# Kernel optimization log

Measured on AMD Instinct MI355X. Metric: run time of the kernel, lower is better.

The kernel has to match this reference:

```python
import jax, jax.numpy as jnp
import numpy as np

N = 100000
E = 3200000
F_IN = 256
F_OUT = 256
HID = 64


def setup_inputs() -> dict:
    key = jax.random.key(0)
    ks = jax.random.split(key, 16)
    stdv = 1.0 / np.sqrt(F_OUT)
    std_att = 1.0 / np.sqrt(HID)
    std_att_vec = 1.0 / np.sqrt(3.0)
    u = lambda k, shape, s: jax.random.uniform(k, shape, jnp.float32, -s, s)
    return {
        "inputx": jax.random.normal(ks[0], (N, F_IN), jnp.float32),
        "row_A": jax.random.randint(ks[1], (E,), 0, N),
        "col_A": jax.random.randint(ks[2], (E,), 0, N),
        "val_A": jax.random.uniform(ks[3], (E,), jnp.float32),
        "row_A2": jax.random.randint(ks[4], (E,), 0, N),
        "col_A2": jax.random.randint(ks[5], (E,), 0, N),
        "val_A2": jax.random.uniform(ks[6], (E,), jnp.float32),
        "weight_A": u(ks[7], (F_IN, F_OUT), stdv),
        "weight_A2": u(ks[8], (F_IN, F_OUT), stdv),
        "weight_mlp": u(ks[9], (F_IN, F_OUT), stdv),
        "W_k0": u(ks[10], (F_OUT, HID), std_att),
        "W_k1": u(ks[11], (F_OUT, HID), std_att),
        "W_k2": u(ks[12], (F_OUT, HID), std_att),
        "att_vec_A": u(ks[13], (F_OUT, HID), std_att),
        "att_vec_A2": u(ks[14], (F_OUT, HID), std_att),
        "att_vec_mlp": u(ks[15], (F_OUT, HID), std_att),
        "att_vec": u(jax.random.fold_in(key, 99), (3, 3), std_att_vec),
    }


def _spmm(row, col, val, x, n):
    # COO sparse-dense matmul: out[r] += val_e * x[c]
    return jax.ops.segment_sum(val[:, None] * x[col], row, num_segments=n)


def reference(inputx, row_A, col_A, val_A, row_A2, col_A2, val_A2,
              weight_A, weight_A2, weight_mlp, W_k0, W_k1, W_k2,
              att_vec_A, att_vec_A2, att_vec_mlp, att_vec):
    n = inputx.shape[0]
    out_A = jax.nn.relu(_spmm(row_A, col_A, val_A, inputx @ weight_A, n))
    out_A2 = jax.nn.relu(_spmm(row_A2, col_A2, val_A2, inputx @ weight_A2, n))
    out_mlp = jax.nn.relu(inputx @ weight_mlp)
    # attention gating
    T = 3.0
    k0 = jnp.mean(out_A @ W_k0, axis=0, keepdims=True)    # [1, HID]
    k1 = jnp.mean(out_A2 @ W_k1, axis=0, keepdims=True)
    k2 = jnp.mean(out_mlp @ W_k2, axis=0, keepdims=True)
    logits = jnp.concatenate([
        (out_A @ att_vec_A) @ k0.T,      # [N, 1]
        (out_A2 @ att_vec_A2) @ k1.T,
        (out_mlp @ att_vec_mlp) @ k2.T,
    ], axis=1)                           # [N, 3]
    att = jax.nn.softmax((jax.nn.sigmoid(logits) @ att_vec) / T, axis=1)
    return 3.0 * (att[:, 0:1] * out_A + att[:, 1:2] * out_A2 + att[:, 2:3] * out_mlp)
```

## Files before the change

### kernel.cpp

```cpp
#include <hip/hip_runtime.h>

typedef __bf16 bf16;
typedef __bf16 bf16x4 __attribute__((ext_vector_type(4)));
typedef __bf16 bf16x8 __attribute__((ext_vector_type(8)));
typedef float f32x4 __attribute__((ext_vector_type(4)));

__device__ __forceinline__ f32x4 bf2f(bf16x4 v){
  f32x4 r; r[0]=(float)v[0]; r[1]=(float)v[1]; r[2]=(float)v[2]; r[3]=(float)v[3]; return r;
}

__device__ __forceinline__ void gload16(const bf16* g, bf16* l){
  __builtin_amdgcn_global_load_lds(
      (const __attribute__((address_space(1))) unsigned int*)(g),
      (__attribute__((address_space(3))) unsigned int*)(l), 16, 0, 0);
}

#define NBMAX 1600
#define NBP   1601
#define CHUNK 16384
#define CAP   2560
#define CSRCAP 2816

__global__ __launch_bounds__(256) void k_xcvt(const float* __restrict__ X, bf16* __restrict__ Xb, int total){
  int i = (blockIdx.x*256 + threadIdx.x)*8;
  if (i + 8 <= total){
    float4 a = *(const float4*)(X+i);
    float4 b = *(const float4*)(X+i+4);
    bf16x8 v;
    v[0]=(bf16)a.x; v[1]=(bf16)a.y; v[2]=(bf16)a.z; v[3]=(bf16)a.w;
    v[4]=(bf16)b.x; v[5]=(bf16)b.y; v[6]=(bf16)b.z; v[7]=(bf16)b.w;
    *(bf16x8*)(Xb+i) = v;
  }
}

__global__ __launch_bounds__(256) void k_wt(const float* __restrict__ W0, const float* __restrict__ W1,
                                            const float* __restrict__ W2, bf16* __restrict__ WT3){
  int n = blockIdx.x, mat = blockIdx.y, k = threadIdx.x;
  const float* W = (mat==0)?W0:((mat==1)?W1:W2);
  WT3[mat*65536 + n*256 + k] = (bf16)W[k*256 + n];
}

__global__ __launch_bounds__(512) void k_binT(const int* __restrict__ rowA, const int* __restrict__ colA,
    const float* __restrict__ valA, const int* __restrict__ rowA2, const int* __restrict__ colA2,
    const float* __restrict__ valA2, int* __restrict__ gcur,
    int2* __restrict__ pTA, int2* __restrict__ pTA2, int E, int NB){
  __shared__ int hist[NBMAX];
  int mat = blockIdx.y;
  const int* row = mat? rowA2 : rowA;
  const int* col = mat? colA2 : colA;
  const float* val = mat? valA2 : valA;
  int2* pT = mat? pTA2 : pTA;
  int t = threadIdx.x;
  for (int i=t; i<NB; i+=512) hist[i] = 0;
  __syncthreads();
  int base = blockIdx.x * CHUNK;
  int endi = base + CHUNK; if (endi > E) endi = E;
  for (int i = base + t; i < endi; i += 512) atomicAdd(&hist[row[i] >> 6], 1);
  __syncthreads();
  for (int i=t; i<NB; i+=512){
    int c = hist[i];
    if (c) hist[i] = i*CAP + atomicAdd(&gcur[mat*NB + i], c);
  }
  __syncthreads();
  for (int i = base + t; i < endi; i += 512){
    int r = row[i];
    int pos = atomicAdd(&hist[r >> 6], 1);
    int2 p; p.x = ((r & 63) << 17) | col[i]; p.y = __float_as_int(val[i]);
    pT[pos] = p;
  }
}

__global__ __launch_bounds__(256) void k_bscan(const int* __restrict__ gcur, int* __restrict__ gstart,
    int NB, int E){
  __shared__ int ss[256];
  __shared__ int carry;
  int mat = blockIdx.x;
  int t = threadIdx.x;
  if (t==0) carry = 0;
  __syncthreads();
  for (int base=0; base<NB; base+=256){
    int i = base + t;
    int v = (i < NB) ? gcur[mat*NB + i] : 0;
    ss[t] = v; __syncthreads();
    for (int off=1; off<256; off<<=1){
      int u = (t>=off)? ss[t-off] : 0;
      __syncthreads();
      ss[t] += u;
      __syncthreads();
    }
    int excl = carry + ss[t] - v;
    if (i < NB) gstart[mat*NBP + i] = excl;
    int tot = ss[255];
    __syncthreads();
    if (t==0) carry += tot;
    __syncthreads();
  }
  if (t==0) gstart[mat*NBP + NB] = E;
}

__global__ __launch_bounds__(256) void k_csr(const int2* __restrict__ pTA, const int2* __restrict__ pTA2,
    const int* __restrict__ gcur, const int* __restrict__ gstart,
    int* __restrict__ rsA, int* __restrict__ rsA2,
    int2* __restrict__ permA, int2* __restrict__ permA2, int N, int NB, int E){
  __shared__ int2 raw[CSRCAP];
  __shared__ unsigned short sidx[CSRCAP];
  __shared__ int fill[64];
  __shared__ int rowst_l[64];
  int mat = blockIdx.y;
  const int2* pT = mat? pTA2 : pTA;
  int2* perm = mat? permA2 : permA;
  int* rs = mat? rsA2 : rsA;
  int b = blockIdx.x;
  int t = threadIdx.x;
  int r0 = b*64;
  int src = b*CAP;
  int cnt = gcur[mat*NB + b];
  if (cnt > CSRCAP) cnt = CSRCAP;
  int dst = gstart[mat*NBP + b];
  if (t < 64) fill[t] = 0;
  __syncthreads();
  for (int i = t; i < cnt; i += 256){
    int2 e = pT[src + i];
    raw[i] = e;
    atomicAdd(&fill[e.x >> 17], 1);
  }
  __syncthreads();
  if (t < 64){
    int v = fill[t];
    int x = v;
#pragma unroll
    for (int off=1; off<64; off<<=1){
      int u = __shfl_up(x, off, 64);
      if (t >= off) x += u;
    }
    int st = x - v;
    rowst_l[t] = st;
    if (r0 + t < N) rs[r0 + t] = dst + st;
    fill[t] = 0;
  }
  __syncthreads();
  for (int i = t; i < cnt; i += 256){
    int rl = raw[i].x >> 17;
    int pos = atomicAdd(&fill[rl], 1);
    sidx[rowst_l[rl] + pos] = (unsigned short)i;
  }
  __syncthreads();
  for (int j = t; j < cnt; j += 256){
    int2 e = raw[sidx[j]];
    int2 o; o.x = e.x & 0x1FFFF; o.y = e.y;
    perm[dst + j] = o;
  }
  if (t == 0 && b == NB-1) rs[N] = E;
}

__global__ __launch_bounds__(256) void k_spmm(const bf16* __restrict__ Xb,
    const int* __restrict__ rsA, const int* __restrict__ rsA2,
    const int2* __restrict__ permA, const int2* __restrict__ permA2,
    bf16* __restrict__ AXb, bf16* __restrict__ A2Xb, int N){
  int mat = blockIdx.y;
  const int* rs = mat? rsA2 : rsA;
  const int2* perm = mat? permA2 : permA;
  bf16* dst = mat? A2Xb : AXb;
  int t = threadIdx.x, lane = t & 63, wv = t >> 6;
  int c = lane*4;
  int rstep = gridDim.x*4;

  for (int row = blockIdx.x*4 + wv; row < N; row += rstep){
    int e = rs[row], eend = rs[row+1];
    f32x4 acc; acc[0]=0.f; acc[1]=0.f; acc[2]=0.f; acc[3]=0.f;

    int2 p0, p1, p2, p3;
    bool have = (e + 3 < eend);
    if (have){ p0 = perm[e]; p1 = perm[e+1]; p2 = perm[e+2]; p3 = perm[e+3]; }
    while (have){
      bf16x4 g0 = *(const bf16x4*)(Xb + (size_t)p0.x*256 + c);
      bf16x4 g1 = *(const bf16x4*)(Xb + (size_t)p1.x*256 + c);
      bf16x4 g2 = *(const bf16x4*)(Xb + (size_t)p2.x*256 + c);
      bf16x4 g3 = *(const bf16x4*)(Xb + (size_t)p3.x*256 + c);
      float v0 = __int_as_float(p0.y), v1 = __int_as_float(p1.y);
      float v2 = __int_as_float(p2.y), v3 = __int_as_float(p3.y);
      e += 4;
      have = (e + 3 < eend);
      if (have){ p0 = perm[e]; p1 = perm[e+1]; p2 = perm[e+2]; p3 = perm[e+3]; }
      acc += v0 * bf2f(g0);
      acc += v1 * bf2f(g1);
      acc += v2 * bf2f(g2);
      acc += v3 * bf2f(g3);
    }
    for (; e < eend; ++e){
      int2 p = perm[e];
      acc += __int_as_float(p.y) * bf2f(*(const bf16x4*)(Xb + (size_t)p.x*256 + c));
    }
    bf16x4 o;
#pragma unroll
    for (int k=0;k<4;k++) o[k] = (bf16)acc[k];
    *(bf16x4*)(dst + (size_t)row*256 + c) = o;
  }
}

__global__ __launch_bounds__(512) void k_gemm(bf16* __restrict__ M0, bf16* __restrict__ M1,
        bf16* __restrict__ M2, const bf16* __restrict__ WT3, float* __restrict__ colsum, int N){
  __shared__ __align__(16) bf16 sA[128*32];
  __shared__ __align__(16) bf16 sB[256*32];
  __shared__ float gcs[256];
  int t = threadIdx.x;
  int lane = t & 63, wave = t>>6, wm = wave>>2, wn = wave&3;
  int mat = blockIdx.y;
  int m0 = blockIdx.x*128;
  const bf16* WT = WT3 + mat*65536;
  bf16* M = (mat==0)?M0:((mat==1)?M1:M2);

  f32x4 acc[4][4];
#pragma unroll
  for (int i=0;i<4;i++)
#pragma unroll
    for (int j=0;j<4;j++){ acc[i][j][0]=0.f; acc[i][j][1]=0.f; acc[i][j][2]=0.f; acc[i][j][3]=0.f; }

  int ar = t>>2, ac = t&3;
  int alc = ac ^ ((ar>>1)&3);
  int agrow = m0 + ar; if (agrow > N-1) agrow = N-1;
  const bf16* gA = M + (size_t)agrow*256 + alc*8;
  bf16* lA = sA + ar*32 + ac*8;

  int br = t>>2, bc = t&3;
  int blc = bc ^ ((br>>1)&3);
  const bf16* gB0 = WT + br*256 + blc*8;
  const bf16* gB1 = WT + (br+128)*256 + blc*8;
  bf16* lB0 = sB + br*32 + bc*8;
  bf16* lB1 = sB + (br+128)*32 + bc*8;

  for (int k0=0; k0<256; k0+=32){
    __syncthreads();
    gload16(gA  + k0, lA);
    gload16(gB0 + k0, lB0);
    gload16(gB1 + k0, lB1);
    __syncthreads();

    bf16x8 af[4], bfr[4];
#pragma unroll
    for (int i=0;i<4;i++){
      int arow = wm*64 + i*16 + (lane&15);
      int pc = (lane>>4) ^ ((arow>>1)&3);
      af[i] = *(const bf16x8*)(sA + arow*32 + pc*8);
    }
#pragma unroll
    for (int j=0;j<4;j++){
      int brow = wn*64 + j*16 + (lane&15);
      int pc = (lane>>4) ^ ((brow>>1)&3);
      bfr[j] = *(const bf16x8*)(sB + brow*32 + pc*8);
    }
#pragma unroll
    for (int i=0;i<4;i++)
#pragma unroll
      for (int j=0;j<4;j++)
        acc[i][j] = __builtin_amdgcn_mfma_f32_16x16x32_bf16(af[i], bfr[j], acc[i][j], 0,0,0);
  }

  int col0 = wn*64 + (lane&15);
  int rb = m0 + wm*64 + ((lane>>4)<<2);
  float pj[4] = {0.f,0.f,0.f,0.f};
#pragma unroll
  for (int i=0;i<4;i++){
#pragma unroll
    for (int tt=0; tt<4; tt++){
      int r = rb + i*16 + tt;
      if (r < N){
#pragma unroll
        for (int j=0;j<4;j++){
          float vv = acc[i][j][tt];
          if (vv < 0.f) vv = 0.f;
          pj[j] += vv;
          M[(size_t)r*256 + col0 + j*16] = (bf16)vv;
        }
      }
    }
  }
  if (t < 256) gcs[t] = 0.f;
  __syncthreads();
#pragma unroll
  for (int j=0;j<4;j++) atomicAdd(&gcs[col0 + j*16], pj[j]);
  __syncthreads();
  if (t < 256) atomicAdd(&colsum[mat*256 + t], gcs[t]);
}

__global__ void k_attn(const float* __restrict__ colsum,
    const float* __restrict__ Wk0, const float* __restrict__ Wk1, const float* __restrict__ Wk2,
    const float* __restrict__ V0, const float* __restrict__ V1, const float* __restrict__ V2,
    float* __restrict__ wvec, int N){
  __shared__ float smean[768];
  __shared__ float sk[192];
  int t = threadIdx.x;
  float invN = 1.f/(float)N;
  smean[t]     = colsum[t]     * invN;
  smean[t+256] = colsum[t+256] * invN;
  smean[t+512] = colsum[t+512] * invN;
  __syncthreads();
  if (t < 192){
    int j = t>>6, h = t&63;
    const float* Wk = (j==0)?Wk0:((j==1)?Wk1:Wk2);
    float s = 0.f;
    for (int cc=0; cc<256; cc++) s += smean[j*256+cc]*Wk[cc*64+h];
    sk[j*64+h] = s;
  }
  __syncthreads();
  int c = t;
  for (int j=0;j<3;j++){
    const float* V = (j==0)?V0:((j==1)?V1:V2);
    float s = 0.f;
    for (int h=0;h<64;h++) s += V[c*64+h]*sk[j*64+h];
    wvec[j*256+c] = s;
  }
}

__global__ __launch_bounds__(256) void k_epi(const bf16* __restrict__ A, const bf16* __restrict__ B,
    const bf16* __restrict__ M, const float* __restrict__ wvec, const float* __restrict__ av9,
    float* __restrict__ out, int N){
  __shared__ float sw[768];
  __shared__ float sav[9];
  int t = threadIdx.x;
  sw[t] = wvec[t]; sw[t+256] = wvec[t+256]; sw[t+512] = wvec[t+512];
  if (t < 9) sav[t] = av9[t];
  __syncthreads();
  int row = blockIdx.x*4 + (t>>6);
  if (row >= N) return;
  int lane = t & 63;
  int c = lane*4;
  f32x4 a = bf2f(*(const bf16x4*)(A + (size_t)row*256 + c));
  f32x4 b = bf2f(*(const bf16x4*)(B + (size_t)row*256 + c));
  f32x4 m = bf2f(*(const bf16x4*)(M + (size_t)row*256 + c));
  float p0 = a[0]*sw[c] + a[1]*sw[c+1] + a[2]*sw[c+2] + a[3]*sw[c+3];
  float p1 = b[0]*sw[256+c] + b[1]*sw[256+c+1] + b[2]*sw[256+c+2] + b[3]*sw[256+c+3];
  float p2 = m[0]*sw[512+c] + m[1]*sw[512+c+1] + m[2]*sw[512+c+2] + m[3]*sw[512+c+3];
#pragma unroll
  for (int off=32; off>=1; off>>=1){
    p0 += __shfl_xor(p0, off);
    p1 += __shfl_xor(p1, off);
    p2 += __shfl_xor(p2, off);
  }
  float s0 = 1.f/(1.f+expf(-p0));
  float s1 = 1.f/(1.f+expf(-p1));
  float s2 = 1.f/(1.f+expf(-p2));
  float g0 = (s0*sav[0] + s1*sav[3] + s2*sav[6]) * (1.f/3.f);
  float g1 = (s0*sav[1] + s1*sav[4] + s2*sav[7]) * (1.f/3.f);
  float g2 = (s0*sav[2] + s1*sav[5] + s2*sav[8]) * (1.f/3.f);
  float mx = fmaxf(g0, fmaxf(g1,g2));
  float e0 = expf(g0-mx), e1 = expf(g1-mx), e2 = expf(g2-mx);
  float inv = 3.f/(e0+e1+e2);
  float a0 = e0*inv, a1 = e1*inv, a2 = e2*inv;
  f32x4 o = a0*a + a1*b + a2*m;
  *(f32x4*)(out + (size_t)row*256 + c) = o;
}

extern "C" void kernel_launch(void* const* d_in, const int* in_sizes, int n_in,
                              void* d_out, int out_size, void* d_ws, size_t ws_size,
                              hipStream_t stream){
  const float* X    = (const float*)d_in[0];
  const int*   rowA = (const int*)d_in[1];
  const int*   colA = (const int*)d_in[2];
  const float* valA = (const float*)d_in[3];
  const int*   rowA2= (const int*)d_in[4];
  const int*   colA2= (const int*)d_in[5];
  const float* valA2= (const float*)d_in[6];
  const float* W0   = (const float*)d_in[7];
  const float* W1   = (const float*)d_in[8];
  const float* W2   = (const float*)d_in[9];
  const float* Wk0  = (const float*)d_in[10];
  const float* Wk1  = (const float*)d_in[11];
  const float* Wk2  = (const float*)d_in[12];
  const float* V0   = (const float*)d_in[13];
  const float* V1   = (const float*)d_in[14];
  const float* V2   = (const float*)d_in[15];
  const float* AV9  = (const float*)d_in[16];
  int N = in_sizes[0] / 256;
  int E = in_sizes[1];
  int NB = (N + 63) >> 6;
  int ebl2 = (E + CHUNK-1)/CHUNK;

  char* ws = (char*)d_ws;
  size_t off = 0;
  auto take = [&](size_t b)->char*{ char* r = ws + off; off = (off + b + 255) & ~(size_t)255; return r; };
  size_t mb = (size_t)N*256*2;
  bf16* WT3  = (bf16*)take((size_t)3*256*256*2);
  bf16* Xb   = (bf16*)take(mb);
  bf16* B1   = (bf16*)take(mb);
  bf16* B2   = (bf16*)take(mb);
  int* rsA    = (int*)take((size_t)(N+1)*4);
  int* rsA2   = (int*)take((size_t)(N+1)*4);
  int* gcur   = (int*)take((size_t)2*NB*4);
  int* gstart = (int*)take((size_t)2*NBP*4);
  float* colsum = (float*)take(768*4);
  float* wvec   = (float*)take(768*4);
  int2* permA  = (int2*)take((size_t)E*8);
  int2* permA2 = (int2*)take((size_t)E*8);
  int2* pTA  = (int2*)B1;
  int2* pTA2 = (int2*)B2;

  hipMemsetAsync(gcur, 0, (size_t)2*NB*4, stream);
  hipMemsetAsync(colsum, 0, 768*4, stream);

  int total = N*256;
  k_xcvt<<<dim3((total/8 + 255)/256),256,0,stream>>>(X, Xb, total);
  k_wt<<<dim3(256,3),256,0,stream>>>(W0,W1,W2,WT3);
  k_binT<<<dim3(ebl2,2),512,0,stream>>>(rowA,colA,valA,rowA2,colA2,valA2,gcur,pTA,pTA2,E,NB);
  k_bscan<<<2,256,0,stream>>>(gcur,gstart,NB,E);
  k_csr<<<dim3(NB,2),256,0,stream>>>(pTA,pTA2,gcur,gstart,rsA,rsA2,permA,permA2,N,NB,E);
  int sblk = (N+31)/32;
  k_spmm<<<dim3(sblk,2),256,0,stream>>>(Xb,rsA,rsA2,permA,permA2,B1,B2,N);
  k_gemm<<<dim3((N+127)/128,3),512,0,stream>>>(B1,B2,Xb,WT3,colsum,N);
  k_attn<<<1,256,0,stream>>>(colsum,Wk0,Wk1,Wk2,V0,V1,V2,wvec,N);
  k_epi<<<dim3((N+3)/4),256,0,stream>>>(B1,B2,Xb,wvec,AV9,(float*)d_out,N);
}
```

Before: 1.048 ms.

## Split SpMM into four half-range launches and use plain LDS stores in GEMM

The single two-matrix SpMM launch becomes four launches, each covering half of the rows for one adjacency matrix. This may change scheduling and cache locality of the gathered rows. Separately, the GEMM tile loads now go through registers with vector global loads and LDS stores instead of direct global-to-LDS loads, which adds register traffic. Both pieces look like experiments and carry a risk of extra launch overhead and slower tile staging.

```diff
diff --git a/kernel.cpp b/kernel.cpp
--- a/kernel.cpp
+++ b/kernel.cpp
@@ -7,12 +7,6 @@
 
 __device__ __forceinline__ f32x4 bf2f(bf16x4 v){
   f32x4 r; r[0]=(float)v[0]; r[1]=(float)v[1]; r[2]=(float)v[2]; r[3]=(float)v[3]; return r;
-}
-
-__device__ __forceinline__ void gload16(const bf16* g, bf16* l){
-  __builtin_amdgcn_global_load_lds(
-      (const __attribute__((address_space(1))) unsigned int*)(g),
-      (__attribute__((address_space(3))) unsigned int*)(l), 16, 0, 0);
 }
 
 #define NBMAX 1600
@@ -154,18 +148,13 @@
 }
 
 __global__ __launch_bounds__(256) void k_spmm(const bf16* __restrict__ Xb,
-    const int* __restrict__ rsA, const int* __restrict__ rsA2,
-    const int2* __restrict__ permA, const int2* __restrict__ permA2,
-    bf16* __restrict__ AXb, bf16* __restrict__ A2Xb, int N){
-  int mat = blockIdx.y;
-  const int* rs = mat? rsA2 : rsA;
-  const int2* perm = mat? permA2 : permA;
-  bf16* dst = mat? A2Xb : AXb;
+    const int* __restrict__ rs, const int2* __restrict__ perm,
+    bf16* __restrict__ dst, int rbeg, int rend){
   int t = threadIdx.x, lane = t & 63, wv = t >> 6;
   int c = lane*4;
   int rstep = gridDim.x*4;
 
-  for (int row = blockIdx.x*4 + wv; row < N; row += rstep){
+  for (int row = rbeg + blockIdx.x*4 + wv; row < rend; row += rstep){
     int e = rs[row], eend = rs[row+1];
     f32x4 acc; acc[0]=0.f; acc[1]=0.f; acc[2]=0.f; acc[3]=0.f;
 
@@ -231,9 +220,9 @@
 
   for (int k0=0; k0<256; k0+=32){
     __syncthreads();
-    gload16(gA  + k0, lA);
-    gload16(gB0 + k0, lB0);
-    gload16(gB1 + k0, lB1);
+    *(bf16x8*)lA  = *(const bf16x8*)(gA  + k0);
+    *(bf16x8*)lB0 = *(const bf16x8*)(gB0 + k0);
+    *(bf16x8*)lB1 = *(const bf16x8*)(gB1 + k0);
     __syncthreads();
 
     bf16x8 af[4], bfr[4];
@@ -404,8 +393,12 @@
   k_binT<<<dim3(ebl2,2),512,0,stream>>>(rowA,colA,valA,rowA2,colA2,valA2,gcur,pTA,pTA2,E,NB);
   k_bscan<<<2,256,0,stream>>>(gcur,gstart,NB,E);
   k_csr<<<dim3(NB,2),256,0,stream>>>(pTA,pTA2,gcur,gstart,rsA,rsA2,permA,permA2,N,NB,E);
-  int sblk = (N+31)/32;
-  k_spmm<<<dim3(sblk,2),256,0,stream>>>(Xb,rsA,rsA2,permA,permA2,B1,B2,N);
+  int half = N/2;
+  int sblk2 = (half + 31)/32;
+  k_spmm<<<dim3(sblk2),256,0,stream>>>(Xb,rsA, permA, B1, 0,    half);
+  k_spmm<<<dim3(sblk2),256,0,stream>>>(Xb,rsA, permA, B1, half, N);
+  k_spmm<<<dim3(sblk2),256,0,stream>>>(Xb,rsA2,permA2,B2, 0,    half);
+  k_spmm<<<dim3(sblk2),256,0,stream>>>(Xb,rsA2,permA2,B2, half, N);
   k_gemm<<<dim3((N+127)/128,3),512,0,stream>>>(B1,B2,Xb,WT3,colsum,N);
   k_attn<<<1,256,0,stream>>>(colsum,Wk0,Wk1,Wk2,V0,V1,V2,wvec,N);
   k_epi<<<dim3((N+3)/4),256,0,stream>>>(B1,B2,Xb,wvec,AV9,(float*)d_out,N);
```

Result: slower. 1.125 ms (+7.3%).
